# Kernel tuning notes

Measured on AMD Instinct MI355X. Metric: run time of the kernel, lower is better.

The kernel has to match this reference:

```python
import jax, jax.numpy as jnp
import numpy as np

B, N, S, D, H = 64, 4096, 8, 256, 512
ITERS = 3
EPS = 1e-8      # slot-attention renormalize epsilon
LN_EPS = 1e-5   # torch LayerNorm default


def _ln(x, g, b):
    m = jnp.mean(x, -1, keepdims=True)
    v = jnp.mean((x - m) ** 2, -1, keepdims=True)
    return (x - m) * jax.lax.rsqrt(v + LN_EPS) * g + b


def setup_inputs() -> dict:
    key = jax.random.key(0)
    ks = jax.random.split(key, 12)

    def xav(k, shape):
        s = (6.0 / (shape[-2] + shape[-1])) ** 0.5
        return jax.random.uniform(k, shape, jnp.float32, -s, s)

    gru_s = 1.0 / (D ** 0.5)
    return {
        "inputs": jax.random.normal(ks[0], (B, N, D), jnp.float32),
        "init_noise": jax.random.normal(ks[1], (B, S, D), jnp.float32),
        "slots_mu": xav(ks[2], (1, 1, D)),
        "slots_log_sigma": xav(ks[3], (1, 1, D)),
        "ln_in_g": jnp.ones(D), "ln_in_b": jnp.zeros(D),
        "ln_slots_g": jnp.ones(D), "ln_slots_b": jnp.zeros(D),
        "ln_mlp_g": jnp.ones(D), "ln_mlp_b": jnp.zeros(D),
        "Wq": xav(ks[4], (D, D)),
        "Wk": xav(ks[5], (D, D)),
        "Wv": xav(ks[6], (D, D)),
        "W_ih": jax.random.uniform(ks[7], (3 * D, D), jnp.float32, -gru_s, gru_s),
        "W_hh": jax.random.uniform(ks[8], (3 * D, D), jnp.float32, -gru_s, gru_s),
        "b_ih": jnp.zeros(3 * D), "b_hh": jnp.zeros(3 * D),
        "W1": xav(ks[9], (H, D)), "b1": jnp.zeros(H),
        "W2": xav(ks[10], (D, H)), "b2": jnp.zeros(D),
    }


def reference(inputs, init_noise, slots_mu, slots_log_sigma,
              ln_in_g, ln_in_b, ln_slots_g, ln_slots_b, ln_mlp_g, ln_mlp_b,
              Wq, Wk, Wv, W_ih, W_hh, b_ih, b_hh, W1, b1, W2, b2):
    x = _ln(inputs, ln_in_g, ln_in_b)               # (B,N,D)
    k = jnp.einsum('bnd,ed->bne', x, Wk)             # (B,N,D)
    v = jnp.einsum('bnd,ed->bne', x, Wv)             # (B,N,D)
    slots = slots_mu + jnp.exp(slots_log_sigma) * init_noise  # (B,S,D)
    scale = D ** (-0.5)
    for _ in range(ITERS):
        prev = slots
        s = _ln(slots, ln_slots_g, ln_slots_b)
        q = jnp.einsum('bsd,ed->bse', s, Wq) * scale
        logits = jnp.einsum('bse,bne->bsn', q, k)    # (B,S,N)
        attn = jax.nn.softmax(logits, -1) + EPS
        attn = attn / jnp.sum(attn, -1, keepdims=True)
        upd = jnp.einsum('bsn,bne->bse', attn, v)    # (B,S,D)
        # GRUCell (torch semantics)
        gx = jnp.einsum('bsd,ed->bse', upd, W_ih) + b_ih
        gh = jnp.einsum('bsd,ed->bse', prev, W_hh) + b_hh
        xr, xz, xn = jnp.split(gx, 3, -1)
        hr, hz, hn = jnp.split(gh, 3, -1)
        r = jax.nn.sigmoid(xr + hr)
        z = jax.nn.sigmoid(xz + hz)
        n = jnp.tanh(xn + r * hn)
        slots = (1.0 - z) * n + z * prev
        # residual MLP
        m = _ln(slots, ln_mlp_g, ln_mlp_b)
        h1 = jax.nn.relu(jnp.einsum('bsd,hd->bsh', m, W1) + b1)
        slots = slots + jnp.einsum('bsh,dh->bsd', h1, W2) + b2
    return slots
```

## Files before the change

### kernel.cpp

```cpp
#include <hip/hip_runtime.h>

#define BB 64
#define NN 4096
#define SS 8
#define DD 256
#define HH 512
#define NCH 8
#define CHK 512
#define LSP 516

typedef __attribute__((ext_vector_type(4))) float f32x4;
typedef __attribute__((ext_vector_type(8))) short short8;
typedef __attribute__((ext_vector_type(8))) __bf16 bf16x8;

static __device__ __forceinline__ f32x4 MFMA(short8 a, short8 b, f32x4 c){
  return __builtin_amdgcn_mfma_f32_16x16x32_bf16(
      __builtin_bit_cast(bf16x8, a), __builtin_bit_cast(bf16x8, b), c, 0, 0, 0);
}

static __device__ __forceinline__ unsigned short f2bf(float f){
  unsigned int x = __builtin_bit_cast(unsigned int, f);
  x += 0x7FFFu + ((x >> 16) & 1u);
  return (unsigned short)(x >> 16);
}

static __device__ __forceinline__ unsigned int pk2(float a, float b){
  return (unsigned int)f2bf(a) | ((unsigned int)f2bf(b) << 16);
}

__global__ __launch_bounds__(256, 4) void pre_kernel(
    const float* __restrict__ Wq, const float* __restrict__ Wk,
    const float* __restrict__ Wih, const float* __restrict__ Wv,
    float* __restrict__ wqkT, float* __restrict__ mf32)
{
  __shared__ float sh[256];
  const int blk = blockIdx.x, t = threadIdx.x;
  if(blk < 256){
    const int d2 = blk;
    sh[t] = Wk[(size_t)t * 256 + d2];
    __syncthreads();
    float acc = 0.f;
    #pragma unroll 8
    for(int e = 0; e < 256; ++e) acc += sh[e] * Wq[(size_t)e * 256 + t];
    wqkT[(size_t)d2 * 256 + t] = acc * 0.0625f;
  } else {
    const int e = blk - 256;
    sh[t] = Wih[(size_t)e * 256 + t];
    __syncthreads();
    float acc = 0.f;
    #pragma unroll 8
    for(int d = 0; d < 256; ++d) acc += sh[d] * Wv[(size_t)d * 256 + t];
    mf32[(size_t)e * 256 + t] = acc;
  }
}

struct PackDesc {
  const float* src[5];
  unsigned short* dst[5];
  int ET[5];
  int K[5];
  int blkStart[6];
};

__global__ void pack_all_kernel(PackDesc pd){
  int blk = blockIdx.x;
  int seg = 0;
  #pragma unroll
  for(int i = 1; i < 5; ++i) if(blk >= pd.blkStart[i]) seg = i;
  int tid = (blk - pd.blkStart[seg]) * 256 + threadIdx.x;
  int ET = pd.ET[seg], K = pd.K[seg];
  if(tid >= ET * 16 * K) return;
  int i    = tid & 7;
  int lane = (tid >> 3) & 63;
  int rest = tid >> 9;
  int et = rest % ET;
  int kk = rest / ET;
  int row = et * 16 + (lane & 15);
  int col = kk * 32 + ((lane >> 4) << 3) + i;
  pd.dst[seg][tid] = f2bf(pd.src[seg][(size_t)row * K + col]);
}

__global__ __launch_bounds__(256, 4) void ln_kernel(
    const float* __restrict__ inp, const float* __restrict__ g, const float* __restrict__ bta,
    unsigned short* __restrict__ x)
{
  const int t = threadIdx.x, w = t >> 6, l = t & 63;
  const size_t row0 = (size_t)blockIdx.x * 64;
  const int li = l & 15, lg = l >> 4;

  float4 gg[4], bb[4];
  #pragma unroll
  for(int q = 0; q < 4; ++q){
    gg[q] = ((const float4*)g)[li + q * 16];
    bb[q] = ((const float4*)bta)[li + q * 16];
  }
  #pragma unroll
  for(int rr = 0; rr < 4; ++rr){
    int r = w * 16 + rr * 4 + lg;
    const float4* rp = (const float4*)(inp + (row0 + r) * DD);
    float4 xv[4];
    #pragma unroll
    for(int q = 0; q < 4; ++q) xv[q] = rp[li + q * 16];
    float s1 = 0.f, s2 = 0.f;
    #pragma unroll
    for(int q = 0; q < 4; ++q){
      s1 += xv[q].x + xv[q].y + xv[q].z + xv[q].w;
      s2 += xv[q].x*xv[q].x + xv[q].y*xv[q].y + xv[q].z*xv[q].z + xv[q].w*xv[q].w;
    }
    #pragma unroll
    for(int o = 8; o >= 1; o >>= 1){ s1 += __shfl_xor(s1, o); s2 += __shfl_xor(s2, o); }
    float mean = s1 * (1.0f/256.0f);
    float inv  = rsqrtf(s2 * (1.0f/256.0f) - mean*mean + 1e-5f);
    #pragma unroll
    for(int q = 0; q < 4; ++q){
      float y0 = (xv[q].x-mean)*inv*gg[q].x + bb[q].x;
      float y1 = (xv[q].y-mean)*inv*gg[q].y + bb[q].y;
      float y2 = (xv[q].z-mean)*inv*gg[q].z + bb[q].z;
      float y3 = (xv[q].w-mean)*inv*gg[q].w + bb[q].w;
      *(uint2*)((char*)x + (row0 + r) * 512 + q * 128 + li * 8) =
          make_uint2(pk2(y0,y1), pk2(y2,y3));
    }
  }
}

__global__ __launch_bounds__(256, 1) void init_kernel(
    const float* __restrict__ noise, const float* __restrict__ mu, const float* __restrict__ lsg,
    const float* __restrict__ lng, const float* __restrict__ lnb,
    const short8* __restrict__ wqkp, float* __restrict__ slots, float* __restrict__ qbuf)
{
  const int b = blockIdx.x, t = threadIdx.x, w = t >> 6, l = t & 63;
  __shared__ float SLN[SS * DD];
  __shared__ unsigned short A1[16 * DD];
  float muv = mu[t];
  float sgv = __expf(lsg[t]);
  #pragma unroll
  for(int s = 0; s < SS; ++s){
    float v = muv + sgv * noise[(size_t)b * 2048 + s * 256 + t];
    slots[(size_t)b * 2048 + s * 256 + t] = v;
    SLN[s * 256 + t] = v;
  }
  __syncthreads();
  float4 g4 = ((const float4*)lng)[l], bb4 = ((const float4*)lnb)[l];
  for(int sh = 0; sh < 2; ++sh){
    int s = w * 2 + sh;
    float4 x4 = ((const float4*)(SLN + s * 256))[l];
    float s1 = x4.x + x4.y + x4.z + x4.w;
    float s2 = x4.x*x4.x + x4.y*x4.y + x4.z*x4.z + x4.w*x4.w;
    #pragma unroll
    for(int o = 32; o >= 1; o >>= 1){ s1 += __shfl_xor(s1, o); s2 += __shfl_xor(s2, o); }
    float mean = s1 * (1.0f/256.0f);
    float inv  = rsqrtf(s2 * (1.0f/256.0f) - mean*mean + 1e-5f);
    float y0 = (x4.x-mean)*inv*g4.x + bb4.x;
    float y1 = (x4.y-mean)*inv*g4.y + bb4.y;
    float y2 = (x4.z-mean)*inv*g4.z + bb4.z;
    float y3 = (x4.w-mean)*inv*g4.w + bb4.w;
    int byte = s * 512 + ((l * 8) ^ ((s & 7) << 4));
    *(uint2*)((char*)A1 + byte) = make_uint2(pk2(y0,y1), pk2(y2,y3));
  }
  __syncthreads();
  const int m = l & 15;
  short8 af[8];
  #pragma unroll
  for(int kk = 0; kk < 8; ++kk){
    int ab = m * 512 + (((kk * 64) + ((l >> 4) << 4)) ^ ((m & 7) << 4));
    af[kk] = *(const short8*)((const char*)A1 + ab);
  }
  #pragma unroll
  for(int i = 0; i < 4; ++i){
    int et = w + i * 4;
    f32x4 c = (f32x4){0,0,0,0};
    #pragma unroll
    for(int kk = 0; kk < 8; ++kk) c = MFMA(af[kk], wqkp[((kk * 16 + et) << 6) + l], c);
    int e = et * 16 + (l & 15);
    #pragma unroll
    for(int j = 0; j < 4; ++j){
      int s = ((l >> 4) << 2) + j;
      if(s < 8) qbuf[(size_t)b * 2048 + s * 256 + e] = c[j];
    }
  }
}

__global__ __launch_bounds__(256, 3) void attn_kernel(
    const unsigned short* __restrict__ x_, const float* __restrict__ qbuf,
    float* __restrict__ pupd, float* __restrict__ pms)
{
  const int blk = blockIdx.x;
  const int b = blk >> 3, c = blk & 7;
  const int t = threadIdx.x, w = t >> 6, l = t & 63;
  __shared__ float ls[8 * LSP];
  __shared__ __align__(16) char xv[256 * 128];

  const int m = l & 15, lg = l >> 4;
  short8 aq[8];
  #pragma unroll
  for(int kk = 0; kk < 8; ++kk){
    if(m < 8){
      const float* qp = qbuf + (size_t)b * 2048 + m * 256 + kk * 32 + (lg << 3);
      float4 qa = *(const float4*)qp;
      float4 qb = *(const float4*)(qp + 4);
      int4 pv = make_int4((int)pk2(qa.x,qa.y), (int)pk2(qa.z,qa.w),
                          (int)pk2(qb.x,qb.y), (int)pk2(qb.z,qb.w));
      aq[kk] = __builtin_bit_cast(short8, pv);
    } else {
      aq[kk] = (short8){0,0,0,0,0,0,0,0};
    }
  }

  const unsigned short* xb = x_ + ((size_t)b * NN + (size_t)c * CHK) * DD;
  #pragma unroll
  for(int nt = 0; nt < 8; ++nt){
    int nb = w * 128 + nt * 16;
    f32x4 acc = (f32x4){0,0,0,0};
    #pragma unroll
    for(int kk = 0; kk < 8; ++kk){
      short8 bk = *(const short8*)(xb + (size_t)(nb + m) * DD + kk * 32 + ((l >> 4) << 3));
      acc = MFMA(aq[kk], bk, acc);
    }
    if(l < 32){
      int s4 = (l >> 4) * 4;
      #pragma unroll
      for(int j = 0; j < 4; ++j) ls[(s4 + j) * LSP + nb + m] = acc[j];
    }
  }
  __syncthreads();

  for(int sh = 0; sh < 2; ++sh){
    int s = w * 2 + sh;
    float* base = ls + s * LSP;
    float4 v0 = *(float4*)(base + l * 4);
    float4 v1 = *(float4*)(base + 256 + l * 4);
    float mx = fmaxf(fmaxf(fmaxf(v0.x,v0.y),fmaxf(v0.z,v0.w)),
                     fmaxf(fmaxf(v1.x,v1.y),fmaxf(v1.z,v1.w)));
    #pragma unroll
    for(int o = 32; o >= 1; o >>= 1) mx = fmaxf(mx, __shfl_xor(mx, o));
    float e0 = __expf(v0.x-mx), e1 = __expf(v0.y-mx), e2 = __expf(v0.z-mx), e3 = __expf(v0.w-mx);
    float e4 = __expf(v1.x-mx), e5 = __expf(v1.y-mx), e6 = __expf(v1.z-mx), e7 = __expf(v1.w-mx);
    float sm = e0+e1+e2+e3+e4+e5+e6+e7;
    #pragma unroll
    for(int o = 32; o >= 1; o >>= 1) sm += __shfl_xor(sm, o);
    *(float4*)(base + l * 4)       = make_float4(e0,e1,e2,e3);
    *(float4*)(base + 256 + l * 4) = make_float4(e4,e5,e6,e7);
    if(l == 0){
      pms[(((size_t)b * 8 + c) * 8 + s) * 2    ] = mx;
      pms[(((size_t)b * 8 + c) * 8 + s) * 2 + 1] = sm;
    }
  }
  __syncthreads();

  short8 pa[16];
  #pragma unroll
  for(int kk = 0; kk < 16; ++kk){
    if(m < 8){
      const float* pp = ls + m * LSP + kk * 32 + ((l >> 4) << 3);
      int4 pv = make_int4((int)pk2(pp[0],pp[1]), (int)pk2(pp[2],pp[3]),
                          (int)pk2(pp[4],pp[5]), (int)pk2(pp[6],pp[7]));
      pa[kk] = __builtin_bit_cast(short8, pv);
    } else {
      pa[kk] = (short8){0,0,0,0,0,0,0,0};
    }
  }

  f32x4 acc[4];
  #pragma unroll
  for(int dt = 0; dt < 4; ++dt) acc[dt] = (f32x4){0,0,0,0};
  const int p = t & 31, db = t >> 5;

  uint4 va0, va1, va2, va3, vb0, vb1, vb2, vb3;
  {
    const unsigned short* rA = xb + (size_t)(2 * p) * DD + db * 32;
    const unsigned short* rB = rA + DD;
    va0 = *(const uint4*)(rA);      vb0 = *(const uint4*)(rB);
    va1 = *(const uint4*)(rA + 8);  vb1 = *(const uint4*)(rB + 8);
    va2 = *(const uint4*)(rA + 16); vb2 = *(const uint4*)(rB + 16);
    va3 = *(const uint4*)(rA + 24); vb3 = *(const uint4*)(rB + 24);
  }

  for(int ng = 0; ng < 8; ++ng){
    {
      uint4 VA[4] = {va0, va1, va2, va3};
      uint4 VB[4] = {vb0, vb1, vb2, vb3};
      #pragma unroll
      for(int q = 0; q < 4; ++q){
        unsigned int wa[4] = {VA[q].x, VA[q].y, VA[q].z, VA[q].w};
        unsigned int wb[4] = {VB[q].x, VB[q].y, VB[q].z, VB[q].w};
        #pragma unroll
        for(int h = 0; h < 4; ++h){
          int d0 = db * 32 + q * 8 + h * 2;
          unsigned int a = wa[h], bv = wb[h];
          unsigned int v0 = (a & 0xFFFFu) | (bv << 16);
          unsigned int v1 = (a >> 16) | (bv & 0xFFFF0000u);
          *(unsigned int*)(xv + d0 * 128 + ((p * 4) ^ ((d0 & 7) << 4))) = v0;
          int d1 = d0 + 1;
          *(unsigned int*)(xv + d1 * 128 + ((p * 4) ^ ((d1 & 7) << 4))) = v1;
        }
      }
    }
    if(ng < 7){
      const unsigned short* rA = xb + (size_t)((ng + 1) * 64 + 2 * p) * DD + db * 32;
      const unsigned short* rB = rA + DD;
      va0 = *(const uint4*)(rA);      vb0 = *(const uint4*)(rB);
      va1 = *(const uint4*)(rA + 8);  vb1 = *(const uint4*)(rB + 8);
      va2 = *(const uint4*)(rA + 16); vb2 = *(const uint4*)(rB + 16);
      va3 = *(const uint4*)(rA + 24); vb3 = *(const uint4*)(rB + 24);
    }
    #pragma unroll
    for(int kkloc = 0; kkloc < 2; ++kkloc){
      int kk = ng * 2 + kkloc;
      #pragma unroll
      for(int dt = 0; dt < 4; ++dt){
        int d = w * 64 + dt * 16 + m;
        short8 bv = *(const short8*)(xv + d * 128 + ((kkloc * 64 + lg * 16) ^ ((d & 7) << 4)));
        acc[dt] = MFMA(pa[kk], bv, acc[dt]);
      }
    }
  }
  if(l < 32){
    int s4 = (l >> 4) * 4;
    #pragma unroll
    for(int dt = 0; dt < 4; ++dt){
      int d0 = w * 64 + dt * 16;
      #pragma unroll
      for(int j = 0; j < 4; ++j)
        pupd[((size_t)b * 8 + c) * 2048 + (s4 + j) * 256 + d0 + m] = acc[dt][j];
    }
  }
}

__global__ __launch_bounds__(1024, 1) void update_kernel(
    const float* __restrict__ pupd, const float* __restrict__ pms,
    float* __restrict__ slots, float* __restrict__ qbuf,
    const short8* __restrict__ mp, const short8* __restrict__ whh,
    const float* __restrict__ bih, const float* __restrict__ bhh,
    const short8* __restrict__ w1p, const float* __restrict__ b1v,
    const short8* __restrict__ w2p, const float* __restrict__ b2v,
    const float* __restrict__ lnsg, const float* __restrict__ lnsb,
    const float* __restrict__ lnmg, const float* __restrict__ lnmb,
    const short8* __restrict__ wqkp,
    float* __restrict__ dout, const int last)
{
  const int b = blockIdx.x, t = threadIdx.x, w = t >> 6, l = t & 63;
  __shared__ unsigned short A1[16 * 256];
  __shared__ unsigned short A2[16 * 256];
  __shared__ unsigned short A3[16 * 512];
  __shared__ float GR[8 * 256], GZ[8 * 256], GXN[8 * 256], GHN[8 * 256];
  __shared__ float SL[8 * 256];
  __shared__ float PMS[128];

  if(t < 128) PMS[t] = pms[(size_t)b * 128 + t];
  __syncthreads();

  const int col = t & 255, sg = t >> 8;
  float upd[2], pv[2];
  #pragma unroll
  for(int ss = 0; ss < 2; ++ss){
    int s = sg * 2 + ss;
    float mx = -1e30f;
    #pragma unroll
    for(int cc = 0; cc < 8; ++cc) mx = fmaxf(mx, PMS[(cc * 8 + s) * 2]);
    float Z = 0.f, u = 0.f;
    #pragma unroll
    for(int cc = 0; cc < 8; ++cc){
      float e = __expf(PMS[(cc * 8 + s) * 2] - mx);
      Z += e * PMS[(cc * 8 + s) * 2 + 1];
      u += e * pupd[((size_t)b * 8 + cc) * 2048 + s * 256 + col];
    }
    upd[ss] = u / Z;
    pv[ss]  = slots[(size_t)b * 2048 + s * 256 + col];
  }
  #pragma unroll
  for(int ss = 0; ss < 2; ++ss){
    int s = sg * 2 + ss;
    int byte = s * 512 + ((col * 2) ^ ((s & 7) << 4));
    *(unsigned short*)((char*)A1 + byte) = f2bf(upd[ss]);
    *(unsigned short*)((char*)A2 + byte) = f2bf(pv[ss]);
  }
  __syncthreads();

  {
    const int mq = l & 15;
    short8 a1f[8], a2f[8];
    #pragma unroll
    for(int kk = 0; kk < 8; ++kk){
      int ab = mq * 512 + (((kk * 64) + ((l >> 4) << 4)) ^ ((mq & 7) << 4));
      a1f[kk] = *(const short8*)((const char*)A1 + ab);
      a2f[kk] = *(const short8*)((const char*)A2 + ab);
    }
    #pragma unroll
    for(int i = 0; i < 3; ++i){
      int et = w + i * 16;
      f32x4 c1 = (f32x4){0,0,0,0}, c2 = (f32x4){0,0,0,0};
      #pragma unroll
      for(int kk = 0; kk < 8; ++kk){
        c1 = MFMA(a1f[kk], mp[((kk * 48 + et) << 6) + l], c1);
        c2 = MFMA(a2f[kk], whh[((kk * 48 + et) << 6) + l], c2);
      }
      int e = et * 16 + (l & 15);
      float xb = bih[e], hb = bhh[e];
      #pragma unroll
      for(int j = 0; j < 4; ++j){
        int s = ((l >> 4) << 2) + j;
        if(s < 8){
          float xx = c1[j] + xb, h = c2[j] + hb;
          if(i == 0)      GR[s * 256 + e      ] = 1.f/(1.f + __expf(-(xx + h)));
          else if(i == 1) GZ[s * 256 + (e-256)] = 1.f/(1.f + __expf(-(xx + h)));
          else { GXN[s * 256 + (e-512)] = xx; GHN[s * 256 + (e-512)] = h; }
        }
      }
    }
  }
  __syncthreads();

  #pragma unroll
  for(int ss = 0; ss < 2; ++ss){
    int s = sg * 2 + ss, idx = s * 256 + col;
    float r = GR[idx], z = GZ[idx], xn = GXN[idx], hn = GHN[idx];
    float nn = tanhf(xn + r * hn);
    SL[idx] = (1.f - z) * nn + z * pv[ss];
  }
  __syncthreads();

  if(w < 8){
    float4 g4 = ((const float4*)lnmg)[l], bb4 = ((const float4*)lnmb)[l];
    int s = w;
    float4 x4 = ((const float4*)(SL + s * 256))[l];
    float s1 = x4.x + x4.y + x4.z + x4.w;
    float s2 = x4.x*x4.x + x4.y*x4.y + x4.z*x4.z + x4.w*x4.w;
    #pragma unroll
    for(int o = 32; o >= 1; o >>= 1){ s1 += __shfl_xor(s1, o); s2 += __shfl_xor(s2, o); }
    float mean = s1 * (1.0f/256.0f);
    float inv  = rsqrtf(s2 * (1.0f/256.0f) - mean*mean + 1e-5f);
    float y0 = (x4.x-mean)*inv*g4.x + bb4.x;
    float y1 = (x4.y-mean)*inv*g4.y + bb4.y;
    float y2 = (x4.z-mean)*inv*g4.z + bb4.z;
    float y3 = (x4.w-mean)*inv*g4.w + bb4.w;
    int byte = s * 512 + ((l * 8) ^ ((s & 7) << 4));
    *(uint2*)((char*)A1 + byte) = make_uint2(pk2(y0,y1), pk2(y2,y3));
  }
  __syncthreads();

  {
    const int mq = l & 15;
    short8 af[8];
    #pragma unroll
    for(int kk = 0; kk < 8; ++kk){
      int ab = mq * 512 + (((kk * 64) + ((l >> 4) << 4)) ^ ((mq & 7) << 4));
      af[kk] = *(const short8*)((const char*)A1 + ab);
    }
    #pragma unroll
    for(int i = 0; i < 2; ++i){
      int et = w + i * 16;
      f32x4 cc = (f32x4){0,0,0,0};
      #pragma unroll
      for(int kk = 0; kk < 8; ++kk) cc = MFMA(af[kk], w1p[((kk * 32 + et) << 6) + l], cc);
      int e = et * 16 + (l & 15);
      float bb = b1v[e];
      #pragma unroll
      for(int j = 0; j < 4; ++j){
        int s = ((l >> 4) << 2) + j;
        if(s < 8){
          float h = fmaxf(cc[j] + bb, 0.f);
          int byte = s * 1024 + ((e * 2) ^ ((s & 7) << 4));
          *(unsigned short*)((char*)A3 + byte) = f2bf(h);
        }
      }
    }
  }
  __syncthreads();

  {
    const int mq = l & 15;
    short8 af[16];
    #pragma unroll
    for(int kk = 0; kk < 16; ++kk){
      int ab = mq * 1024 + (((kk * 64) + ((l >> 4) << 4)) ^ ((mq & 7) << 4));
      af[kk] = *(const short8*)((const char*)A3 + ab);
    }
    {
      int et = w;
      f32x4 cc = (f32x4){0,0,0,0};
      #pragma unroll
      for(int kk = 0; kk < 16; ++kk) cc = MFMA(af[kk], w2p[((kk * 16 + et) << 6) + l], cc);
      int e = et * 16 + (l & 15);
      float bb = b2v[e];
      #pragma unroll
      for(int j = 0; j < 4; ++j){
        int s = ((l >> 4) << 2) + j;
        if(s < 8) GR[s * 256 + e] = SL[s * 256 + e] + cc[j] + bb;
      }
    }
  }
  __syncthreads();

  for(int i = t; i < 2048; i += 1024){
    float v = GR[i];
    slots[(size_t)b * 2048 + i] = v;
    if(last) dout[(size_t)b * 2048 + i] = v;
  }
  if(w < 8){
    float4 g4 = ((const float4*)lnsg)[l], bb4 = ((const float4*)lnsb)[l];
    int s = w;
    float4 x4 = ((const float4*)(GR + s * 256))[l];
    float s1 = x4.x + x4.y + x4.z + x4.w;
    float s2 = x4.x*x4.x + x4.y*x4.y + x4.z*x4.z + x4.w*x4.w;
    #pragma unroll
    for(int o = 32; o >= 1; o >>= 1){ s1 += __shfl_xor(s1, o); s2 += __shfl_xor(s2, o); }
    float mean = s1 * (1.0f/256.0f);
    float inv  = rsqrtf(s2 * (1.0f/256.0f) - mean*mean + 1e-5f);
    float y0 = (x4.x-mean)*inv*g4.x + bb4.x;
    float y1 = (x4.y-mean)*inv*g4.y + bb4.y;
    float y2 = (x4.z-mean)*inv*g4.z + bb4.z;
    float y3 = (x4.w-mean)*inv*g4.w + bb4.w;
    int byte = s * 512 + ((l * 8) ^ ((s & 7) << 4));
    *(uint2*)((char*)A1 + byte) = make_uint2(pk2(y0,y1), pk2(y2,y3));
  }
  __syncthreads();
  {
    const int mq = l & 15;
    short8 af[8];
    #pragma unroll
    for(int kk = 0; kk < 8; ++kk){
      int ab = mq * 512 + (((kk * 64) + ((l >> 4) << 4)) ^ ((mq & 7) << 4));
      af[kk] = *(const short8*)((const char*)A1 + ab);
    }
    {
      int et = w;
      f32x4 cc = (f32x4){0,0,0,0};
      #pragma unroll
      for(int kk = 0; kk < 8; ++kk) cc = MFMA(af[kk], wqkp[((kk * 16 + et) << 6) + l], cc);
      int e = et * 16 + (l & 15);
      #pragma unroll
      for(int j = 0; j < 4; ++j){
        int s = ((l >> 4) << 2) + j;
        if(s < 8) qbuf[(size_t)b * 2048 + s * 256 + e] = cc[j];
      }
    }
  }
}

extern "C" void kernel_launch(void* const* d_in, const int* in_sizes, int n_in,
                              void* d_out, int out_size, void* d_ws, size_t ws_size,
                              hipStream_t stream)
{
  const float* inp   = (const float*)d_in[0];
  const float* noise = (const float*)d_in[1];
  const float* mu    = (const float*)d_in[2];
  const float* lsg   = (const float*)d_in[3];
  const float* lngi  = (const float*)d_in[4];
  const float* lnbi  = (const float*)d_in[5];
  const float* lngs  = (const float*)d_in[6];
  const float* lnbs  = (const float*)d_in[7];
  const float* lngm  = (const float*)d_in[8];
  const float* lnbm  = (const float*)d_in[9];
  const float* Wq    = (const float*)d_in[10];
  const float* Wk    = (const float*)d_in[11];
  const float* Wv    = (const float*)d_in[12];
  const float* Wih   = (const float*)d_in[13];
  const float* Whh   = (const float*)d_in[14];
  const float* bih   = (const float*)d_in[15];
  const float* bhh   = (const float*)d_in[16];
  const float* W1    = (const float*)d_in[17];
  const float* b1    = (const float*)d_in[18];
  const float* W2    = (const float*)d_in[19];
  const float* b2    = (const float*)d_in[20];
  float* dout = (float*)d_out;

  char* ws = (char*)d_ws;
  size_t off = 0;
  unsigned short* x   = (unsigned short*)(ws + off); off += (size_t)BB*NN*DD*2;
  short8* wqkp= (short8*)(ws + off); off += (size_t)256*256*2;
  short8* mp  = (short8*)(ws + off); off += (size_t)768*256*2;
  short8* whhp= (short8*)(ws + off); off += (size_t)768*256*2;
  short8* w1p = (short8*)(ws + off); off += (size_t)512*256*2;
  short8* w2p = (short8*)(ws + off); off += (size_t)256*512*2;
  float* wqkT = (float*)(ws + off);  off += (size_t)256*256*4;
  float* mf32 = (float*)(ws + off);  off += (size_t)768*256*4;
  float* qbuf = (float*)(ws + off);  off += (size_t)512*256*4;
  float* slots= (float*)(ws + off);  off += (size_t)512*256*4;
  float* pupd = (float*)(ws + off);  off += (size_t)64*8*8*256*4;
  float* pms  = (float*)(ws + off);  off += (size_t)64*8*8*2*4;

  pre_kernel<<<1024, 256, 0, stream>>>(Wq, Wk, Wih, Wv, wqkT, mf32);

  PackDesc pd;
  const float* srcs[5] = {wqkT, mf32, Whh, W1, W2};
  unsigned short* dsts[5] = {(unsigned short*)wqkp, (unsigned short*)mp,
                             (unsigned short*)whhp, (unsigned short*)w1p,
                             (unsigned short*)w2p};
  int ets[5] = {16, 48, 48, 32, 16};
  int ks [5] = {256, 256, 256, 256, 512};
  int cum = 0;
  for(int i = 0; i < 5; ++i){
    pd.src[i] = srcs[i]; pd.dst[i] = dsts[i]; pd.ET[i] = ets[i]; pd.K[i] = ks[i];
    pd.blkStart[i] = cum;
    cum += (ets[i] * 16 * ks[i] + 255) / 256;
  }
  pd.blkStart[5] = cum;
  pack_all_kernel<<<cum, 256, 0, stream>>>(pd);

  ln_kernel<<<4096, 256, 0, stream>>>(inp, lngi, lnbi, x);
  init_kernel<<<64, 256, 0, stream>>>(noise, mu, lsg, lngs, lnbs, wqkp, slots, qbuf);

  for(int it = 0; it < 3; ++it){
    attn_kernel<<<512, 256, 0, stream>>>(x, qbuf, pupd, pms);
    update_kernel<<<64, 1024, 0, stream>>>(pupd, pms, slots, qbuf, mp, whhp,
        bih, bhh, w1p, b1, w2p, b2, lngs, lnbs, lngm, lnbm, wqkp, dout, (it == 2) ? 1 : 0);
  }
}
```

Before: 342.3 us.

## Split attention into 16 chunks per batch with aliased shared memory and MFMA priority

Halves the sequence chunk each attention block handles (256 instead of 512 tokens), doubling the grid to 1024 blocks. The logits buffer and the transposed-V staging buffer now share one 32 KB shared-memory region, with an extra barrier between them. This cuts LDS use per block and should raise occupancy. s_setprio is raised around the MFMA section, and the update kernel merges 16 partial softmax/update results instead of 8. The cost is twice the partial-result traffic and the merge work in update_kernel, plus an extra sync.

Measured after the change: 338.2 us (median of 2 runs). About the same (-1.2%).

```diff
diff --git a/kernel.cpp b/kernel.cpp
--- a/kernel.cpp
+++ b/kernel.cpp
@@ -5,9 +5,9 @@
 #define SS 8
 #define DD 256
 #define HH 512
-#define NCH 8
-#define CHK 512
-#define LSP 516
+#define NCH 16
+#define CHK 256
+#define LSP2 260
 
 typedef __attribute__((ext_vector_type(4))) float f32x4;
 typedef __attribute__((ext_vector_type(8))) short short8;
@@ -185,10 +185,11 @@
     float* __restrict__ pupd, float* __restrict__ pms)
 {
   const int blk = blockIdx.x;
-  const int b = blk >> 3, c = blk & 7;
+  const int b = blk >> 4, c = blk & 15;
   const int t = threadIdx.x, w = t >> 6, l = t & 63;
-  __shared__ float ls[8 * LSP];
-  __shared__ __align__(16) char xv[256 * 128];
+  __shared__ __align__(16) char SMEM[32768];
+  float* ls = (float*)SMEM;
+  char*  xv = SMEM;
 
   const int m = l & 15, lg = l >> 4;
   short8 aq[8];
@@ -208,50 +209,46 @@
 
   const unsigned short* xb = x_ + ((size_t)b * NN + (size_t)c * CHK) * DD;
   #pragma unroll
-  for(int nt = 0; nt < 8; ++nt){
-    int nb = w * 128 + nt * 16;
+  for(int nt = 0; nt < 4; ++nt){
+    int nb = w * 64 + nt * 16;
     f32x4 acc = (f32x4){0,0,0,0};
     #pragma unroll
     for(int kk = 0; kk < 8; ++kk){
-      short8 bk = *(const short8*)(xb + (size_t)(nb + m) * DD + kk * 32 + ((l >> 4) << 3));
+      short8 bk = *(const short8*)(xb + (size_t)(nb + m) * DD + kk * 32 + (lg << 3));
       acc = MFMA(aq[kk], bk, acc);
     }
     if(l < 32){
-      int s4 = (l >> 4) * 4;
-      #pragma unroll
-      for(int j = 0; j < 4; ++j) ls[(s4 + j) * LSP + nb + m] = acc[j];
+      int s4 = lg * 4;
+      #pragma unroll
+      for(int j = 0; j < 4; ++j) ls[(s4 + j) * LSP2 + nb + m] = acc[j];
     }
   }
   __syncthreads();
 
   for(int sh = 0; sh < 2; ++sh){
     int s = w * 2 + sh;
-    float* base = ls + s * LSP;
+    float* base = ls + s * LSP2;
     float4 v0 = *(float4*)(base + l * 4);
-    float4 v1 = *(float4*)(base + 256 + l * 4);
-    float mx = fmaxf(fmaxf(fmaxf(v0.x,v0.y),fmaxf(v0.z,v0.w)),
-                     fmaxf(fmaxf(v1.x,v1.y),fmaxf(v1.z,v1.w)));
+    float mx = fmaxf(fmaxf(v0.x,v0.y),fmaxf(v0.z,v0.w));
     #pragma unroll
     for(int o = 32; o >= 1; o >>= 1) mx = fmaxf(mx, __shfl_xor(mx, o));
     float e0 = __expf(v0.x-mx), e1 = __expf(v0.y-mx), e2 = __expf(v0.z-mx), e3 = __expf(v0.w-mx);
-    float e4 = __expf(v1.x-mx), e5 = __expf(v1.y-mx), e6 = __expf(v1.z-mx), e7 = __expf(v1.w-mx);
-    float sm = e0+e1+e2+e3+e4+e5+e6+e7;
+    float sm = e0+e1+e2+e3;
     #pragma unroll
     for(int o = 32; o >= 1; o >>= 1) sm += __shfl_xor(sm, o);
-    *(float4*)(base + l * 4)       = make_float4(e0,e1,e2,e3);
-    *(float4*)(base + 256 + l * 4) = make_float4(e4,e5,e6,e7);
+    *(float4*)(base + l * 4) = make_float4(e0,e1,e2,e3);
     if(l == 0){
-      pms[(((size_t)b * 8 + c) * 8 + s) * 2    ] = mx;
-      pms[(((size_t)b * 8 + c) * 8 + s) * 2 + 1] = sm;
-    }
-  }
-  __syncthreads();
-
-  short8 pa[16];
-  #pragma unroll
-  for(int kk = 0; kk < 16; ++kk){
+      pms[(((size_t)b * 16 + c) * 8 + s) * 2    ] = mx;
+      pms[(((size_t)b * 16 + c) * 8 + s) * 2 + 1] = sm;
+    }
+  }
+  __syncthreads();
+
+  short8 pa[8];
+  #pragma unroll
+  for(int kk = 0; kk < 8; ++kk){
     if(m < 8){
-      const float* pp = ls + m * LSP + kk * 32 + ((l >> 4) << 3);
+      const float* pp = ls + m * LSP2 + kk * 32 + (lg << 3);
       int4 pv = make_int4((int)pk2(pp[0],pp[1]), (int)pk2(pp[2],pp[3]),
                           (int)pk2(pp[4],pp[5]), (int)pk2(pp[6],pp[7]));
       pa[kk] = __builtin_bit_cast(short8, pv);
@@ -259,6 +256,7 @@
       pa[kk] = (short8){0,0,0,0,0,0,0,0};
     }
   }
+  __syncthreads();
 
   f32x4 acc[4];
   #pragma unroll
@@ -275,7 +273,7 @@
     va3 = *(const uint4*)(rA + 24); vb3 = *(const uint4*)(rB + 24);
   }
 
-  for(int ng = 0; ng < 8; ++ng){
+  for(int ng = 0; ng < 4; ++ng){
     {
       uint4 VA[4] = {va0, va1, va2, va3};
       uint4 VB[4] = {vb0, vb1, vb2, vb3};
@@ -295,7 +293,7 @@
         }
       }
     }
-    if(ng < 7){
+    if(ng < 3){
       const unsigned short* rA = xb + (size_t)((ng + 1) * 64 + 2 * p) * DD + db * 32;
       const unsigned short* rB = rA + DD;
       va0 = *(const uint4*)(rA);      vb0 = *(const uint4*)(rB);
@@ -303,6 +301,7 @@
       va2 = *(const uint4*)(rA + 16); vb2 = *(const uint4*)(rB + 16);
       va3 = *(const uint4*)(rA + 24); vb3 = *(const uint4*)(rB + 24);
     }
+    __builtin_amdgcn_s_setprio(1);
     #pragma unroll
     for(int kkloc = 0; kkloc < 2; ++kkloc){
       int kk = ng * 2 + kkloc;
@@ -313,15 +312,16 @@
         acc[dt] = MFMA(pa[kk], bv, acc[dt]);
       }
     }
+    __builtin_amdgcn_s_setprio(0);
   }
   if(l < 32){
-    int s4 = (l >> 4) * 4;
+    int s4 = lg * 4;
     #pragma unroll
     for(int dt = 0; dt < 4; ++dt){
       int d0 = w * 64 + dt * 16;
       #pragma unroll
       for(int j = 0; j < 4; ++j)
-        pupd[((size_t)b * 8 + c) * 2048 + (s4 + j) * 256 + d0 + m] = acc[dt][j];
+        pupd[((size_t)b * 16 + c) * 2048 + (s4 + j) * 256 + d0 + m] = acc[dt][j];
     }
   }
 }
@@ -344,9 +344,9 @@
   __shared__ unsigned short A3[16 * 512];
   __shared__ float GR[8 * 256], GZ[8 * 256], GXN[8 * 256], GHN[8 * 256];
   __shared__ float SL[8 * 256];
-  __shared__ float PMS[128];
-
-  if(t < 128) PMS[t] = pms[(size_t)b * 128 + t];
+  __shared__ float PMS[256];
+
+  if(t < 256) PMS[t] = pms[(size_t)b * 256 + t];
   __syncthreads();
 
   const int col = t & 255, sg = t >> 8;
@@ -356,13 +356,13 @@
     int s = sg * 2 + ss;
     float mx = -1e30f;
     #pragma unroll
-    for(int cc = 0; cc < 8; ++cc) mx = fmaxf(mx, PMS[(cc * 8 + s) * 2]);
+    for(int cc = 0; cc < 16; ++cc) mx = fmaxf(mx, PMS[(cc * 8 + s) * 2]);
     float Z = 0.f, u = 0.f;
     #pragma unroll
-    for(int cc = 0; cc < 8; ++cc){
+    for(int cc = 0; cc < 16; ++cc){
       float e = __expf(PMS[(cc * 8 + s) * 2] - mx);
       Z += e * PMS[(cc * 8 + s) * 2 + 1];
-      u += e * pupd[((size_t)b * 8 + cc) * 2048 + s * 256 + col];
+      u += e * pupd[((size_t)b * 16 + cc) * 2048 + s * 256 + col];
     }
     upd[ss] = u / Z;
     pv[ss]  = slots[(size_t)b * 2048 + s * 256 + col];
@@ -576,8 +576,8 @@
   float* mf32 = (float*)(ws + off);  off += (size_t)768*256*4;
   float* qbuf = (float*)(ws + off);  off += (size_t)512*256*4;
   float* slots= (float*)(ws + off);  off += (size_t)512*256*4;
-  float* pupd = (float*)(ws + off);  off += (size_t)64*8*8*256*4;
-  float* pms  = (float*)(ws + off);  off += (size_t)64*8*8*2*4;
+  float* pupd = (float*)(ws + off);  off += (size_t)BB*NCH*2048*4;
+  float* pms  = (float*)(ws + off);  off += (size_t)BB*NCH*8*2*4;
 
   pre_kernel<<<1024, 256, 0, stream>>>(Wq, Wk, Wih, Wv, wqkT, mf32);
 
@@ -601,7 +601,7 @@
   init_kernel<<<64, 256, 0, stream>>>(noise, mu, lsg, lngs, lnbs, wqkp, slots, qbuf);
 
   for(int it = 0; it < 3; ++it){
-    attn_kernel<<<512, 256, 0, stream>>>(x, qbuf, pupd, pms);
+    attn_kernel<<<BB * NCH, 256, 0, stream>>>(x, qbuf, pupd, pms);
     update_kernel<<<64, 1024, 0, stream>>>(pupd, pms, slots, qbuf, mp, whhp,
         bih, bhh, w1p, b1, w2p, b2, lngs, lnbs, lngm, lnbm, wqkp, dout, (it == 2) ? 1 : 0);
   }
```
